# Kernel tuning notes

Measured on AMD Instinct MI355X. Metric: run time of the kernel, lower is better.

## Reference

```python
import jax, jax.numpy as jnp
import numpy as np

TEAM = 5
N_PLAYER = 131072
PD = 256
HD = 256
MLP_H = 512
B = 16384

def _combine(t=TEAM):
    i1, i2 = [], []
    for i in range(t):
        for j in range(t):
            if i != j:
                i1.append(i); i2.append(j)
    return np.array(i1), np.array(i2)

IDX1, IDX2 = _combine()

def setup_inputs() -> dict:
    key = jax.random.key(0)
    ks = jax.random.split(key, 12)
    def xavier(k, shape):
        fan_in, fan_out = shape[1], shape[0]
        std = np.sqrt(2.0 / (fan_in + fan_out))
        return (jax.random.normal(k, shape, dtype=jnp.float32) * std)
    return {
        'team_ids': jax.random.randint(ks[0], (B, TEAM), 0, N_PLAYER),
        'emb': xavier(ks[1], (N_PLAYER, PD)),
        'fm_w1': xavier(ks[2], (2 * HD, PD)),
        'fm_b1': jnp.zeros((2 * HD,), jnp.float32),
        'fm_w2': xavier(ks[3], (HD, 2 * HD)),
        'fm_b2': jnp.zeros((HD,), jnp.float32),
        'att_w': xavier(ks[4], (HD, HD)),
        'att_b': jnp.zeros((HD,), jnp.float32),
        'mlp_w1': xavier(ks[5], (MLP_H, HD)),
        'mlp_b1': jnp.zeros((MLP_H,), jnp.float32),
        'mlp_w2': xavier(ks[6], (1, MLP_H)),
        'mlp_b2': jnp.zeros((1,), jnp.float32),
    }

def reference(team_ids, emb, fm_w1, fm_b1, fm_w2, fm_b2, att_w, att_b,
              mlp_w1, mlp_b1, mlp_w2, mlp_b2):
    # embedding lookup: [B, 5, PD]
    x = emb[team_ids]
    # feature mapper: Linear -> SiLU -> Linear  => [B, 5, HD]
    h = jax.nn.silu(jnp.einsum('btp,hp->bth', x, fm_w1) + fm_b1)
    h = jnp.einsum('bth,oh->bto', h, fm_w2) + fm_b2
    # pairwise gather (20 ordered pairs): [B, 20, HD]
    a = h[:, IDX1]
    b = h[:, IDX2]
    prod = a * b
    # small MLP (dropout is inference identity): [B, 20]
    m = jax.nn.silu(jnp.einsum('bph,mh->bpm', prod, mlp_w1) + mlp_b1)
    order2 = (jnp.einsum('bpm,om->bpo', m, mlp_w2) + mlp_b2)[..., 0]
    # attention (reduce=True -> view [B, 5, 4, HD], softmax over axis 2)
    wa = jnp.einsum('bph,oh->bpo', a, att_w) + att_b
    score = (wa * b).sum(-1).reshape(-1, TEAM, TEAM - 1)
    normal = jax.nn.softmax(score, axis=2).reshape(-1, TEAM * (TEAM - 1))
    order2 = order2 * normal
    return order2.sum(axis=1, keepdims=True)  # [B, 1]
```

## Files before the change

### kernel.cpp

```cpp
#include <hip/hip_runtime.h>

#define NB     16384
#define TEAM   5
#define NPAIR  20
#define UPAIR  10
#define PD     256
#define HD     256
#define H1D    512
#define NPLAY  (NB*TEAM)
#define NCHUNK 4

typedef __attribute__((ext_vector_type(4))) float f32x4;
typedef __attribute__((ext_vector_type(8))) short s16x8;

__device__ __forceinline__ float silu_f(float x){ return x / (1.0f + __expf(-x)); }

__device__ __forceinline__ unsigned short bf16_rne(float x){
  unsigned u = __float_as_uint(x);
  unsigned r = u + 0x7fffu + ((u >> 16) & 1u);
  return (unsigned short)(r >> 16);
}
__device__ __forceinline__ float bf16_to_f(unsigned short s){
  return __uint_as_float(((unsigned)s) << 16);
}

__global__ void k_pack(const float* __restrict__ w, short* __restrict__ wf,
                       int KT, int total)
{
  const int tid = blockIdx.x * 256 + threadIdx.x;
  if (tid >= total) return;
  const int slot = tid & 7;
  const int lane = (tid >> 3) & 63;
  const int grp  = tid >> 9;
  const int kt   = grp % KT;
  const int nt   = grp / KT;
  const int K    = KT * 32;
  const int n = nt * 16 + (lane & 15);
  const int k = kt * 32 + ((lane >> 4) << 3) + slot;
  const float v = w[(size_t)n * K + k];
  const unsigned short hi = bf16_rne(v);
  const float lo = v - bf16_to_f(hi);
  wf[tid]         = (short)hi;
  wf[total + tid] = (short)bf16_rne(lo);
}

__global__ __launch_bounds__(256) void k_l1(
    const int* __restrict__ tids, const float* __restrict__ emb,
    const short* __restrict__ w1f, const float* __restrict__ b1,
    float* __restrict__ Hh1)
{
  __shared__ short Af[2*5*2*512];
  __shared__ float Bb[256];
  __shared__ int   Tid[80];

  const int t = threadIdx.x, lane = t & 63, w = t >> 6;
  const int bx = blockIdx.x, cy = blockIdx.y;
  const int p0 = bx * 80;

  if (t < 80) Tid[t] = tids[p0 + t];
  Bb[t] = b1[cy * 256 + t];

  f32x4 acc[5][4];
  #pragma unroll
  for (int mt = 0; mt < 5; ++mt)
    #pragma unroll
    for (int j = 0; j < 4; ++j) acc[mt][j] = (f32x4){0.f,0.f,0.f,0.f};

  const s16x8* Bh = reinterpret_cast<const s16x8*>(w1f);

  for (int kt = 0; kt < 8; ++kt) {
    const int kc = kt >> 1, ks = kt & 1;
    if (ks == 0) {
      __syncthreads();
      const int kt0 = kc * 64;
      #pragma unroll
      for (int f = 0; f < 5; ++f) {
        const int idx4  = t + f * 256;
        const int sg    = (idx4 & 1) * 4;
        const int lane_ = (idx4 >> 1) & 63;
        const int ks_   = (idx4 >> 7) & 1;
        const int mt_   = idx4 >> 8;
        const int p     = mt_ * 16 + (lane_ & 15);
        const int k     = kt0 + ks_ * 32 + ((lane_ >> 4) << 3) + sg;
        const int row   = Tid[p];
        const float4 a4 = *reinterpret_cast<const float4*>(emb + (size_t)row * PD + k);
        float pv[4] = {a4.x, a4.y, a4.z, a4.w};
        short hi[4], lo[4];
        #pragma unroll
        for (int e = 0; e < 4; ++e) {
          const unsigned short h = bf16_rne(pv[e]);
          hi[e] = (short)h;
          lo[e] = (short)bf16_rne(pv[e] - bf16_to_f(h));
        }
        const int aoff = (mt_ * 2 + ks_) * 512 + lane_ * 8 + sg;
        *reinterpret_cast<short4*>(&Af[aoff])        = make_short4(hi[0],hi[1],hi[2],hi[3]);
        *reinterpret_cast<short4*>(&Af[5120 + aoff]) = make_short4(lo[0],lo[1],lo[2],lo[3]);
      }
      __syncthreads();
    }

    s16x8 ah[5], al[5];
    #pragma unroll
    for (int mt = 0; mt < 5; ++mt) {
      ah[mt] = *reinterpret_cast<const s16x8*>(&Af[(mt*2 + ks)*512 + lane*8]);
      al[mt] = *reinterpret_cast<const s16x8*>(&Af[5120 + (mt*2 + ks)*512 + lane*8]);
    }
    #pragma unroll
    for (int j = 0; j < 4; ++j) {
      const int nt = cy * 16 + w * 4 + j;
      const s16x8 bh = Bh[(nt*8 + kt)*64 + lane];
      const s16x8 bl = Bh[16384 + (nt*8 + kt)*64 + lane];
      #pragma unroll
      for (int mt = 0; mt < 5; ++mt) {
        acc[mt][j] = __builtin_amdgcn_mfma_f32_16x16x32_bf16(ah[mt], bh, acc[mt][j], 0,0,0);
        acc[mt][j] = __builtin_amdgcn_mfma_f32_16x16x32_bf16(al[mt], bh, acc[mt][j], 0,0,0);
        acc[mt][j] = __builtin_amdgcn_mfma_f32_16x16x32_bf16(ah[mt], bl, acc[mt][j], 0,0,0);
      }
    }
  }

  #pragma unroll
  for (int mt = 0; mt < 5; ++mt)
    #pragma unroll
    for (int j = 0; j < 4; ++j) {
      const int nl = w * 64 + j * 16 + (lane & 15);
      const int n  = cy * 256 + nl;
      #pragma unroll
      for (int r = 0; r < 4; ++r) {
        const int p = p0 + mt*16 + ((lane >> 4) << 2) + r;
        Hh1[(size_t)p * H1D + n] = silu_f(acc[mt][j][r] + Bb[nl]);
      }
    }
}

__global__ __launch_bounds__(256) void k_l2(
    const float* __restrict__ Hh1, const short* __restrict__ w2f,
    const float* __restrict__ b2, float* __restrict__ Hout)
{
  __shared__ short Af[2*5*2*512];
  __shared__ float Bb[256];

  const int t = threadIdx.x, lane = t & 63, w = t >> 6;
  const int bx = blockIdx.x;
  const int p0 = bx * 80;

  Bb[t] = b2[t];

  f32x4 acc[5][4];
  #pragma unroll
  for (int mt = 0; mt < 5; ++mt)
    #pragma unroll
    for (int j = 0; j < 4; ++j) acc[mt][j] = (f32x4){0.f,0.f,0.f,0.f};

  const s16x8* B2 = reinterpret_cast<const s16x8*>(w2f);

  for (int kt = 0; kt < 16; ++kt) {
    const int kc = kt >> 1, ks = kt & 1;
    if (ks == 0) {
      __syncthreads();
      const int kt0 = kc * 64;
      #pragma unroll
      for (int f = 0; f < 5; ++f) {
        const int idx4  = t + f * 256;
        const int sg    = (idx4 & 1) * 4;
        const int lane_ = (idx4 >> 1) & 63;
        const int ks_   = (idx4 >> 7) & 1;
        const int mt_   = idx4 >> 8;
        const int p     = p0 + mt_ * 16 + (lane_ & 15);
        const int k     = kt0 + ks_ * 32 + ((lane_ >> 4) << 3) + sg;
        const float4 a4 = *reinterpret_cast<const float4*>(Hh1 + (size_t)p * H1D + k);
        float pv[4] = {a4.x, a4.y, a4.z, a4.w};
        short hi[4], lo[4];
        #pragma unroll
        for (int e = 0; e < 4; ++e) {
          const unsigned short h = bf16_rne(pv[e]);
          hi[e] = (short)h;
          lo[e] = (short)bf16_rne(pv[e] - bf16_to_f(h));
        }
        const int aoff = (mt_ * 2 + ks_) * 512 + lane_ * 8 + sg;
        *reinterpret_cast<short4*>(&Af[aoff])        = make_short4(hi[0],hi[1],hi[2],hi[3]);
        *reinterpret_cast<short4*>(&Af[5120 + aoff]) = make_short4(lo[0],lo[1],lo[2],lo[3]);
      }
      __syncthreads();
    }

    s16x8 ah[5], al[5];
    #pragma unroll
    for (int mt = 0; mt < 5; ++mt) {
      ah[mt] = *reinterpret_cast<const s16x8*>(&Af[(mt*2 + ks)*512 + lane*8]);
      al[mt] = *reinterpret_cast<const s16x8*>(&Af[5120 + (mt*2 + ks)*512 + lane*8]);
    }
    #pragma unroll
    for (int j = 0; j < 4; ++j) {
      const int nt = w * 4 + j;
      const s16x8 bh = B2[(nt*16 + kt)*64 + lane];
      const s16x8 bl = B2[16384 + (nt*16 + kt)*64 + lane];
      #pragma unroll
      for (int mt = 0; mt < 5; ++mt) {
        acc[mt][j] = __builtin_amdgcn_mfma_f32_16x16x32_bf16(ah[mt], bh, acc[mt][j], 0,0,0);
        acc[mt][j] = __builtin_amdgcn_mfma_f32_16x16x32_bf16(al[mt], bh, acc[mt][j], 0,0,0);
        acc[mt][j] = __builtin_amdgcn_mfma_f32_16x16x32_bf16(ah[mt], bl, acc[mt][j], 0,0,0);
      }
    }
  }

  #pragma unroll
  for (int mt = 0; mt < 5; ++mt)
    #pragma unroll
    for (int j = 0; j < 4; ++j) {
      const int n = w * 64 + j * 16 + (lane & 15);
      #pragma unroll
      for (int r = 0; r < 4; ++r) {
        const int p = p0 + mt*16 + ((lane >> 4) << 2) + r;
        Hout[(size_t)p * PD + n] = acc[mt][j][r] + Bb[n];
      }
    }
}

__global__ __launch_bounds__(256) void k_fm4(
    const int* __restrict__ tids, const float* __restrict__ emb,
    const short* __restrict__ w1f, const float* __restrict__ b1,
    const short* __restrict__ w2f, const float* __restrict__ b2,
    float* __restrict__ Hout)
{
  __shared__ char smem[65536 + 3072];
  short* Af  = reinterpret_cast<short*>(smem);
  short* H1f = reinterpret_cast<short*>(smem);
  float* Bb  = reinterpret_cast<float*>(smem + 65536);

  const int t = threadIdx.x, lane = t & 63, w = t >> 6;
  const int m0 = blockIdx.x * 32;

  Bb[t]       = b1[t];
  Bb[t + 256] = b1[t + 256];
  Bb[t + 512] = b2[t];

  #pragma unroll
  for (int f = 0; f < 8; ++f) {
    const int g     = t + f * 256;
    const int sg    = (g & 1) * 4;
    const int lane_ = (g >> 1) & 63;
    const int kt_   = (g >> 7) & 7;
    const int mt_   = g >> 10;
    const int p     = mt_ * 16 + (lane_ & 15);
    const int k     = kt_ * 32 + ((lane_ >> 4) << 3) + sg;
    const int row   = tids[m0 + p];
    const float4 a4 = *reinterpret_cast<const float4*>(emb + (size_t)row * PD + k);
    float pv[4] = {a4.x, a4.y, a4.z, a4.w};
    short hi[4], lo[4];
    #pragma unroll
    for (int e = 0; e < 4; ++e) {
      const unsigned short h = bf16_rne(pv[e]);
      hi[e] = (short)h;
      lo[e] = (short)bf16_rne(pv[e] - bf16_to_f(h));
    }
    const int off = ((mt_*8 + kt_)*64 + lane_)*8 + sg;
    *reinterpret_cast<short4*>(&Af[off])        = make_short4(hi[0],hi[1],hi[2],hi[3]);
    *reinterpret_cast<short4*>(&Af[8192 + off]) = make_short4(lo[0],lo[1],lo[2],lo[3]);
  }
  __syncthreads();

  const s16x8* B1 = reinterpret_cast<const s16x8*>(w1f);
  const s16x8* B2 = reinterpret_cast<const s16x8*>(w2f);

  f32x4 acc1[2][8];
  #pragma unroll
  for (int mt = 0; mt < 2; ++mt)
    #pragma unroll
    for (int j = 0; j < 8; ++j) acc1[mt][j] = (f32x4){0.f,0.f,0.f,0.f};

  #pragma unroll
  for (int kt = 0; kt < 8; ++kt) {
    s16x8 ah[2], al[2];
    #pragma unroll
    for (int mt = 0; mt < 2; ++mt) {
      ah[mt] = *reinterpret_cast<const s16x8*>(&Af[((mt*8 + kt)*64 + lane)*8]);
      al[mt] = *reinterpret_cast<const s16x8*>(&Af[8192 + ((mt*8 + kt)*64 + lane)*8]);
    }
    #pragma unroll
    for (int j = 0; j < 8; ++j) {
      const int nt = w * 8 + j;
      const s16x8 bh = B1[(nt*8 + kt)*64 + lane];
      const s16x8 bl = B1[16384 + (nt*8 + kt)*64 + lane];
      #pragma unroll
      for (int mt = 0; mt < 2; ++mt) {
        acc1[mt][j] = __builtin_amdgcn_mfma_f32_16x16x32_bf16(ah[mt], bh, acc1[mt][j], 0,0,0);
        acc1[mt][j] = __builtin_amdgcn_mfma_f32_16x16x32_bf16(al[mt], bh, acc1[mt][j], 0,0,0);
        acc1[mt][j] = __builtin_amdgcn_mfma_f32_16x16x32_bf16(ah[mt], bl, acc1[mt][j], 0,0,0);
      }
    }
  }
  __syncthreads();

  #pragma unroll
  for (int mt = 0; mt < 2; ++mt)
    #pragma unroll
    for (int j = 0; j < 8; ++j) {
      const int n     = w * 128 + j * 16 + (lane & 15);
      const int kt2   = n >> 5;
      const int lhalf = 16 * ((n >> 3) & 3);
      const int slot2 = n & 7;
      #pragma unroll
      for (int r = 0; r < 4; ++r) {
        const int prow = ((lane >> 4) << 2) + r;
        const float v = silu_f(acc1[mt][j][r] + Bb[n]);
        const unsigned short hi = bf16_rne(v);
        const int off = ((mt*16 + kt2)*64 + lhalf + prow)*8 + slot2;
        H1f[off]         = (short)hi;
        H1f[16384 + off] = (short)bf16_rne(v - bf16_to_f(hi));
      }
    }
  __syncthreads();

  f32x4 acc2[2][4];
  #pragma unroll
  for (int mt = 0; mt < 2; ++mt)
    #pragma unroll
    for (int j = 0; j < 4; ++j) acc2[mt][j] = (f32x4){0.f,0.f,0.f,0.f};

  #pragma unroll
  for (int kt = 0; kt < 16; ++kt) {
    s16x8 ah[2], al[2];
    #pragma unroll
    for (int mt = 0; mt < 2; ++mt) {
      ah[mt] = *reinterpret_cast<const s16x8*>(&H1f[((mt*16 + kt)*64 + lane)*8]);
      al[mt] = *reinterpret_cast<const s16x8*>(&H1f[16384 + ((mt*16 + kt)*64 + lane)*8]);
    }
    #pragma unroll
    for (int j = 0; j < 4; ++j) {
      const int nt = w * 4 + j;
      const s16x8 bh = B2[(nt*16 + kt)*64 + lane];
      const s16x8 bl = B2[16384 + (nt*16 + kt)*64 + lane];
      #pragma unroll
      for (int mt = 0; mt < 2; ++mt) {
        acc2[mt][j] = __builtin_amdgcn_mfma_f32_16x16x32_bf16(ah[mt], bh, acc2[mt][j], 0,0,0);
        acc2[mt][j] = __builtin_amdgcn_mfma_f32_16x16x32_bf16(al[mt], bh, acc2[mt][j], 0,0,0);
        acc2[mt][j] = __builtin_amdgcn_mfma_f32_16x16x32_bf16(ah[mt], bl, acc2[mt][j], 0,0,0);
      }
    }
  }

  #pragma unroll
  for (int mt = 0; mt < 2; ++mt)
    #pragma unroll
    for (int j = 0; j < 4; ++j) {
      const int n = w * 64 + j * 16 + (lane & 15);
      #pragma unroll
      for (int r = 0; r < 4; ++r) {
        const int p = m0 + mt*16 + ((lane >> 4) << 2) + r;
        Hout[(size_t)p * PD + n] = acc2[mt][j][r] + Bb[512 + n];
      }
    }
}

__global__ __launch_bounds__(256) void k_score(
    const float* __restrict__ Hin, const short* __restrict__ attf,
    const float* __restrict__ attb, float* __restrict__ SC)
{
  __shared__ char smem[49152 + 1024];
  short* Hf  = reinterpret_cast<short*>(smem);
  float* WAl = reinterpret_cast<float*>(smem);
  float* Ab  = reinterpret_cast<float*>(smem + 49152);

  const int t = threadIdx.x, lane = t & 63, w = t >> 6;
  const int b0 = blockIdx.x * 8;
  const float* src = Hin + (size_t)b0 * TEAM * PD;

  Ab[t] = attb[t];

  #pragma unroll
  for (int f = 0; f < 12; ++f) {
    const int g     = t + f * 256;
    const int sg    = (g & 1) * 4;
    const int lane_ = (g >> 1) & 63;
    const int kt_   = (g >> 7) & 7;
    const int mt_   = g >> 10;
    const int p     = mt_ * 16 + (lane_ & 15);
    const int k     = kt_ * 32 + ((lane_ >> 4) << 3) + sg;
    float4 a4 = make_float4(0.f, 0.f, 0.f, 0.f);
    if (p < 40) a4 = *reinterpret_cast<const float4*>(src + (size_t)p * PD + k);
    float pv[4] = {a4.x, a4.y, a4.z, a4.w};
    short hi[4], lo[4];
    #pragma unroll
    for (int e = 0; e < 4; ++e) {
      const unsigned short h = bf16_rne(pv[e]);
      hi[e] = (short)h;
      lo[e] = (short)bf16_rne(pv[e] - bf16_to_f(h));
    }
    const int off = ((mt_*8 + kt_)*64 + lane_)*8 + sg;
    *reinterpret_cast<short4*>(&Hf[off])         = make_short4(hi[0],hi[1],hi[2],hi[3]);
    *reinterpret_cast<short4*>(&Hf[12288 + off]) = make_short4(lo[0],lo[1],lo[2],lo[3]);
  }
  __syncthreads();

  f32x4 acc[3][4];
  #pragma unroll
  for (int mt = 0; mt < 3; ++mt)
    #pragma unroll
    for (int j = 0; j < 4; ++j) acc[mt][j] = (f32x4){0.f,0.f,0.f,0.f};

  const s16x8* Bh = reinterpret_cast<const s16x8*>(attf);
  #pragma unroll
  for (int kt = 0; kt < 8; ++kt) {
    s16x8 ah[3], al[3];
    #pragma unroll
    for (int mt = 0; mt < 3; ++mt) {
      ah[mt] = *reinterpret_cast<const s16x8*>(&Hf[((mt*8 + kt)*64 + lane)*8]);
      al[mt] = *reinterpret_cast<const s16x8*>(&Hf[12288 + ((mt*8 + kt)*64 + lane)*8]);
    }
    #pragma unroll
    for (int j = 0; j < 4; ++j) {
      const int nt = w * 4 + j;
      const s16x8 bh = Bh[(nt*8 + kt)*64 + lane];
      const s16x8 bl = Bh[8192 + (nt*8 + kt)*64 + lane];
      #pragma unroll
      for (int mt = 0; mt < 3; ++mt) {
        acc[mt][j] = __builtin_amdgcn_mfma_f32_16x16x32_bf16(ah[mt], bh, acc[mt][j], 0,0,0);
        acc[mt][j] = __builtin_amdgcn_mfma_f32_16x16x32_bf16(al[mt], bh, acc[mt][j], 0,0,0);
        acc[mt][j] = __builtin_amdgcn_mfma_f32_16x16x32_bf16(ah[mt], bl, acc[mt][j], 0,0,0);
      }
    }
  }
  __syncthreads();

  #pragma unroll
  for (int mt = 0; mt < 3; ++mt)
    #pragma unroll
    for (int j = 0; j < 4; ++j) {
      const int n = w * 64 + j * 16 + (lane & 15);
      #pragma unroll
      for (int r = 0; r < 4; ++r) {
        const int row = mt * 16 + ((lane >> 4) << 2) + r;
        if (row < 40) WAl[row * 260 + n] = acc[mt][j][r] + Ab[n];
      }
    }
  __syncthreads();

  #pragma unroll
  for (int qq = 0; qq < 2; ++qq) {
    const int q = w * 2 + qq;
    #pragma unroll
    for (int p = 0; p < NPAIR; ++p) {
      const int i1 = p >> 2, jj = p & 3;
      const int i2 = jj + (jj >= i1 ? 1 : 0);
      const float4 a4 = *reinterpret_cast<const float4*>(WAl + (q*TEAM + i1) * 260 + lane * 4);
      const float4 b4 = *reinterpret_cast<const float4*>(src + (size_t)(q*TEAM + i2) * PD + lane * 4);
      float v = a4.x*b4.x + a4.y*b4.y + a4.z*b4.z + a4.w*b4.w;
      #pragma unroll
      for (int off = 32; off > 0; off >>= 1) v += __shfl_xor(v, off);
      if (lane == 0) SC[(size_t)(b0 + q) * NPAIR + p] = v;
    }
  }
}

__global__ __launch_bounds__(256) void k_mlp(
    const float* __restrict__ Hin, const short* __restrict__ w1f,
    const float* __restrict__ b1, const float* __restrict__ w2,
    float* __restrict__ PART)
{
  __shared__ float Hl[40*260];
  __shared__ short Af[2*5*2*512];
  __shared__ float Wb[128];
  __shared__ float Ww[128];

  const int t    = threadIdx.x;
  const int lane = t & 63;
  const int w    = t >> 6;
  const int blkx = blockIdx.x;
  const int cy   = blockIdx.y;
  const int b0   = blkx * 8;

  {
    const float* src = Hin + (size_t)b0 * TEAM * PD;
    #pragma unroll
    for (int rep = 0; rep < 10; ++rep) {
      const int flat = t + rep * 256;
      const int row = flat >> 6, c4 = (flat & 63) * 4;
      *reinterpret_cast<float4*>(Hl + row * 260 + c4) =
        *reinterpret_cast<const float4*>(src + (size_t)row * PD + c4);
    }
    if (t < 128) { Wb[t] = b1[cy * 128 + t]; Ww[t] = w2[cy * 128 + t]; }
  }

  f32x4 acc[5][2];
  #pragma unroll
  for (int mt = 0; mt < 5; ++mt)
    #pragma unroll
    for (int j = 0; j < 2; ++j) acc[mt][j] = (f32x4){0.f,0.f,0.f,0.f};

  const s16x8* Bh = reinterpret_cast<const s16x8*>(w1f);
  const s16x8* Bl = reinterpret_cast<const s16x8*>(w1f + 131072);
  const int nt0 = cy * 8 + w * 2;

  for (int kt = 0; kt < 8; ++kt) {
    const int kc = kt >> 1, ks = kt & 1;
    if (ks == 0) {
      __syncthreads();
      const int kt0 = kc * 64;
      #pragma unroll
      for (int f = 0; f < 5; ++f) {
        const int idx4  = t + f * 256;
        const int sg    = (idx4 & 1) * 4;
        const int lane_ = (idx4 >> 1) & 63;
        const int ks_   = (idx4 >> 7) & 1;
        const int mt_   = idx4 >> 8;
        const int m  = lane_ & 15;
        const int r  = mt_ * 16 + m;
        const int q  = r / UPAIR;
        const int p  = r - q * UPAIR;
        const int i1 = (p >= 4) + (p >= 7) + (p >= 9);
        const int i2 = p - (i1 * (9 - i1)) / 2 + i1 + 1;
        const int kk = kt0 + ks_ * 32 + ((lane_ >> 4) << 3) + sg;
        const float4 a4 = *reinterpret_cast<const float4*>(Hl + (q*TEAM + i1)*260 + kk);
        const float4 b4 = *reinterpret_cast<const float4*>(Hl + (q*TEAM + i2)*260 + kk);
        float pv[4] = {a4.x*b4.x, a4.y*b4.y, a4.z*b4.z, a4.w*b4.w};
        short hi[4], lo[4];
        #pragma unroll
        for (int e = 0; e < 4; ++e) {
          const unsigned short h = bf16_rne(pv[e]);
          hi[e] = (short)h;
          lo[e] = (short)bf16_rne(pv[e] - bf16_to_f(h));
        }
        const int aoff = (mt_ * 2 + ks_) * 512 + lane_ * 8 + sg;
        *reinterpret_cast<short4*>(&Af[aoff])        = make_short4(hi[0],hi[1],hi[2],hi[3]);
        *reinterpret_cast<short4*>(&Af[5120 + aoff]) = make_short4(lo[0],lo[1],lo[2],lo[3]);
      }
      __syncthreads();
    }

    s16x8 ah[5], al[5];
    #pragma unroll
    for (int mt = 0; mt < 5; ++mt) {
      ah[mt] = *reinterpret_cast<const s16x8*>(&Af[(mt*2 + ks)*512 + lane*8]);
      al[mt] = *reinterpret_cast<const s16x8*>(&Af[5120 + (mt*2 + ks)*512 + lane*8]);
    }
    s16x8 bh[2], bl[2];
    #pragma unroll
    for (int j = 0; j < 2; ++j) {
      bh[j] = Bh[((nt0 + j)*8 + kt)*64 + lane];
      bl[j] = Bl[((nt0 + j)*8 + kt)*64 + lane];
    }
    #pragma unroll
    for (int mt = 0; mt < 5; ++mt)
      #pragma unroll
      for (int j = 0; j < 2; ++j) {
        acc[mt][j] = __builtin_amdgcn_mfma_f32_16x16x32_bf16(ah[mt], bh[j], acc[mt][j], 0,0,0);
        acc[mt][j] = __builtin_amdgcn_mfma_f32_16x16x32_bf16(ah[mt], bl[j], acc[mt][j], 0,0,0);
        acc[mt][j] = __builtin_amdgcn_mfma_f32_16x16x32_bf16(al[mt], bh[j], acc[mt][j], 0,0,0);
      }
  }

  __syncthreads();
  float* red = reinterpret_cast<float*>(Af);

  const int colbase = (w * 2) * 16 + (lane & 15);
  #pragma unroll
  for (int mt = 0; mt < 5; ++mt)
    #pragma unroll
    for (int r = 0; r < 4; ++r) {
      float s = 0.0f;
      #pragma unroll
      for (int j = 0; j < 2; ++j) {
        const int c = colbase + j * 16;
        s += silu_f(acc[mt][j][r] + Wb[c]) * Ww[c];
      }
      s += __shfl_xor(s, 1); s += __shfl_xor(s, 2);
      s += __shfl_xor(s, 4); s += __shfl_xor(s, 8);
      if ((lane & 15) == 0) {
        const int row = mt * 16 + ((lane >> 4) << 2) + r;
        red[row * 4 + w] = s;
      }
    }
  __syncthreads();
  if (t < 80) {
    const float s = red[t*4] + red[t*4+1] + red[t*4+2] + red[t*4+3];
    PART[(size_t)cy * (NB*UPAIR) + (size_t)blkx * 80 + t] = s;
  }
}

__global__ void k_final(const float* __restrict__ SC, const float* __restrict__ PART,
                        const float* __restrict__ mb2, float* __restrict__ out)
{
  const int b = blockIdx.x * 256 + threadIdx.x;
  if (b >= NB) return;
  const float bias2 = mb2[0];
  float ord[UPAIR];
  #pragma unroll
  for (int u = 0; u < UPAIR; ++u) {
    float s = bias2;
    #pragma unroll
    for (int g = 0; g < NCHUNK; ++g) s += PART[(size_t)g * (NB*UPAIR) + (size_t)b * UPAIR + u];
    ord[u] = s;
  }
  float sc[NPAIR];
  #pragma unroll
  for (int p = 0; p < NPAIR; ++p) sc[p] = SC[(size_t)b * NPAIR + p];

  float res = 0.0f;
  #pragma unroll
  for (int i = 0; i < TEAM; ++i) {
    float m = sc[4*i];
    #pragma unroll
    for (int jj = 1; jj < 4; ++jj) m = fmaxf(m, sc[4*i + jj]);
    float e[4], d = 0.0f;
    #pragma unroll
    for (int jj = 0; jj < 4; ++jj) { e[jj] = __expf(sc[4*i + jj] - m); d += e[jj]; }
    const float inv = 1.0f / d;
    #pragma unroll
    for (int jj = 0; jj < 4; ++jj) {
      const int i2 = jj + (jj >= i ? 1 : 0);
      const int a  = i < i2 ? i : i2;
      const int bb = i < i2 ? i2 : i;
      const int u  = (a * (9 - a)) / 2 + (bb - a - 1);
      res += ord[u] * e[jj] * inv;
    }
  }
  out[b] = res;
}

extern "C" void kernel_launch(void* const* d_in, const int* in_sizes, int n_in,
                              void* d_out, int out_size, void* d_ws, size_t ws_size,
                              hipStream_t stream)
{
  (void)in_sizes; (void)n_in; (void)out_size;
  const int*   tids = (const int*)  d_in[0];
  const float* emb  = (const float*)d_in[1];
  const float* fw1  = (const float*)d_in[2];
  const float* fb1  = (const float*)d_in[3];
  const float* fw2  = (const float*)d_in[4];
  const float* fb2  = (const float*)d_in[5];
  const float* attw = (const float*)d_in[6];
  const float* attb = (const float*)d_in[7];
  const float* mw1  = (const float*)d_in[8];
  const float* mb1  = (const float*)d_in[9];
  const float* mw2  = (const float*)d_in[10];
  const float* mb2  = (const float*)d_in[11];
  float* out = (float*)d_out;

  float* H     = (float*)d_ws;
  float* SC    = H + (size_t)NPLAY * PD;
  float* PART  = SC + (size_t)NB * NPAIR;
  short* w1f_m = (short*)(PART + (size_t)NCHUNK * NB * UPAIR);
  short* w1f_f = w1f_m + 262144;
  short* w2f_f = w1f_f + 262144;
  short* attf  = w2f_f + 262144;
  float* Hh1   = (float*)(attf + 131072);
  const size_t NEED = (size_t)((char*)(Hh1 + (size_t)NPLAY * H1D) - (char*)d_ws);

  k_pack<<<512, 256, 0, stream>>>(mw1, w1f_m, 8, 131072);
  k_pack<<<512, 256, 0, stream>>>(fw1, w1f_f, 8, 131072);
  k_pack<<<512, 256, 0, stream>>>(fw2, w2f_f, 16, 131072);
  k_pack<<<256, 256, 0, stream>>>(attw, attf, 8, 65536);

  if (ws_size >= NEED) {
    k_l1<<<dim3(NPLAY/80, 2), 256, 0, stream>>>(tids, emb, w1f_f, fb1, Hh1);
    k_l2<<<NPLAY/80, 256, 0, stream>>>(Hh1, w2f_f, fb2, H);
  } else {
    k_fm4<<<NPLAY/32, 256, 0, stream>>>(tids, emb, w1f_f, fb1, w2f_f, fb2, H);
  }
  k_score<<<NB/8, 256, 0, stream>>>(H, attf, attb, SC);
  k_mlp<<<dim3(NB/8, NCHUNK), 256, 0, stream>>>(H, w1f_m, mb1, mw2, PART);
  k_final<<<NB/256, 256, 0, stream>>>(SC, PART, mb2, out);
}
```

Baseline: 660.5 us.

## Compute full MLP hidden width per block instead of splitting into four chunks

The MLP kernel no longer splits the 512-wide hidden layer across four grid-y blocks. Each block now computes all 512 columns, with each wave covering 128 columns through 8 accumulator tiles. The point is to build the hi/lo bf16 pair-product A tiles once instead of four times and to skip the partial-sum reduction across chunks. In exchange register pressure rises (40 f32x4 accumulators per lane), there are four times fewer blocks, and launch bounds now ask for two blocks per CU, which may cause spills.

```diff
diff --git a/kernel.cpp b/kernel.cpp
--- a/kernel.cpp
+++ b/kernel.cpp
@@ -8,7 +8,7 @@
 #define HD     256
 #define H1D    512
 #define NPLAY  (NB*TEAM)
-#define NCHUNK 4
+#define NCHUNK 1
 
 typedef __attribute__((ext_vector_type(4))) float f32x4;
 typedef __attribute__((ext_vector_type(8))) short s16x8;
@@ -453,21 +453,20 @@
   }
 }
 
-__global__ __launch_bounds__(256) void k_mlp(
+__global__ __launch_bounds__(256, 2) void k_mlp(
     const float* __restrict__ Hin, const short* __restrict__ w1f,
     const float* __restrict__ b1, const float* __restrict__ w2,
     float* __restrict__ PART)
 {
   __shared__ float Hl[40*260];
   __shared__ short Af[2*5*2*512];
-  __shared__ float Wb[128];
-  __shared__ float Ww[128];
+  __shared__ float Wb[512];
+  __shared__ float Ww[512];
 
   const int t    = threadIdx.x;
   const int lane = t & 63;
   const int w    = t >> 6;
   const int blkx = blockIdx.x;
-  const int cy   = blockIdx.y;
   const int b0   = blkx * 8;
 
   {
@@ -479,18 +478,21 @@
       *reinterpret_cast<float4*>(Hl + row * 260 + c4) =
         *reinterpret_cast<const float4*>(src + (size_t)row * PD + c4);
     }
-    if (t < 128) { Wb[t] = b1[cy * 128 + t]; Ww[t] = w2[cy * 128 + t]; }
-  }
-
-  f32x4 acc[5][2];
+    Wb[t]       = b1[t];
+    Wb[t + 256] = b1[t + 256];
+    Ww[t]       = w2[t];
+    Ww[t + 256] = w2[t + 256];
+  }
+
+  f32x4 acc[5][8];
   #pragma unroll
   for (int mt = 0; mt < 5; ++mt)
     #pragma unroll
-    for (int j = 0; j < 2; ++j) acc[mt][j] = (f32x4){0.f,0.f,0.f,0.f};
+    for (int j = 0; j < 8; ++j) acc[mt][j] = (f32x4){0.f,0.f,0.f,0.f};
 
   const s16x8* Bh = reinterpret_cast<const s16x8*>(w1f);
   const s16x8* Bl = reinterpret_cast<const s16x8*>(w1f + 131072);
-  const int nt0 = cy * 8 + w * 2;
+  const int nt0 = w * 8;
 
   for (int kt = 0; kt < 8; ++kt) {
     const int kc = kt >> 1, ks = kt & 1;
@@ -534,33 +536,30 @@
       ah[mt] = *reinterpret_cast<const s16x8*>(&Af[(mt*2 + ks)*512 + lane*8]);
       al[mt] = *reinterpret_cast<const s16x8*>(&Af[5120 + (mt*2 + ks)*512 + lane*8]);
     }
-    s16x8 bh[2], bl[2];
-    #pragma unroll
-    for (int j = 0; j < 2; ++j) {
-      bh[j] = Bh[((nt0 + j)*8 + kt)*64 + lane];
-      bl[j] = Bl[((nt0 + j)*8 + kt)*64 + lane];
-    }
-    #pragma unroll
-    for (int mt = 0; mt < 5; ++mt)
-      #pragma unroll
-      for (int j = 0; j < 2; ++j) {
-        acc[mt][j] = __builtin_amdgcn_mfma_f32_16x16x32_bf16(ah[mt], bh[j], acc[mt][j], 0,0,0);
-        acc[mt][j] = __builtin_amdgcn_mfma_f32_16x16x32_bf16(ah[mt], bl[j], acc[mt][j], 0,0,0);
-        acc[mt][j] = __builtin_amdgcn_mfma_f32_16x16x32_bf16(al[mt], bh[j], acc[mt][j], 0,0,0);
-      }
+    #pragma unroll
+    for (int j = 0; j < 8; ++j) {
+      const s16x8 bh = Bh[((nt0 + j)*8 + kt)*64 + lane];
+      const s16x8 bl = Bl[((nt0 + j)*8 + kt)*64 + lane];
+      #pragma unroll
+      for (int mt = 0; mt < 5; ++mt) {
+        acc[mt][j] = __builtin_amdgcn_mfma_f32_16x16x32_bf16(ah[mt], bh, acc[mt][j], 0,0,0);
+        acc[mt][j] = __builtin_amdgcn_mfma_f32_16x16x32_bf16(ah[mt], bl, acc[mt][j], 0,0,0);
+        acc[mt][j] = __builtin_amdgcn_mfma_f32_16x16x32_bf16(al[mt], bh, acc[mt][j], 0,0,0);
+      }
+    }
   }
 
   __syncthreads();
   float* red = reinterpret_cast<float*>(Af);
 
-  const int colbase = (w * 2) * 16 + (lane & 15);
+  const int colbase = w * 128 + (lane & 15);
   #pragma unroll
   for (int mt = 0; mt < 5; ++mt)
     #pragma unroll
     for (int r = 0; r < 4; ++r) {
       float s = 0.0f;
       #pragma unroll
-      for (int j = 0; j < 2; ++j) {
+      for (int j = 0; j < 8; ++j) {
         const int c = colbase + j * 16;
         s += silu_f(acc[mt][j][r] + Wb[c]) * Ww[c];
       }
@@ -574,7 +573,7 @@
   __syncthreads();
   if (t < 80) {
     const float s = red[t*4] + red[t*4+1] + red[t*4+2] + red[t*4+3];
-    PART[(size_t)cy * (NB*UPAIR) + (size_t)blkx * 80 + t] = s;
+    PART[(size_t)blkx * 80 + t] = s;
   }
 }
 
@@ -659,6 +658,6 @@
     k_fm4<<<NPLAY/32, 256, 0, stream>>>(tids, emb, w1f_f, fb1, w2f_f, fb2, H);
   }
   k_score<<<NB/8, 256, 0, stream>>>(H, attf, attb, SC);
-  k_mlp<<<dim3(NB/8, NCHUNK), 256, 0, stream>>>(H, w1f_m, mb1, mw2, PART);
+  k_mlp<<<dim3(NB/8), 256, 0, stream>>>(H, w1f_m, mb1, mw2, PART);
   k_final<<<NB/256, 256, 0, stream>>>(SC, PART, mb2, out);
 }
```

Result: faster. 606.2 us (-8.2%).
